# Performance work log

Hardware: AMD Instinct MI355X
Metric: run time of the kernel (lower is better)

## Reference

```python
import jax, jax.numpy as jnp
import numpy as np

N_NODES = 50000

def _sage_conv(x, src, dst, W_l, b_l, W_r):
    # mean-aggregate neighbor features: messages x[src] summed into dst
    msgs = x[src]                                   # [E, d]
    agg = jax.ops.segment_sum(msgs, dst, num_segments=N_NODES)  # [N, d]
    ones = jnp.ones((src.shape[0],), dtype=x.dtype)
    cnt = jax.ops.segment_sum(ones, dst, num_segments=N_NODES)  # [N]
    agg = agg / jnp.maximum(cnt, 1.0)[:, None]
    return agg @ W_l + b_l + x @ W_r


def setup_inputs() -> dict:
    key = jax.random.key(0)
    ks = jax.random.split(key, 8)
    d_in, hid, out = 64, 128, 64
    x = jax.random.normal(ks[0], (N_NODES, d_in), dtype=jnp.float32)
    edge_index = jax.random.randint(ks[1], (2, 1600000), 0, N_NODES, dtype=jnp.int64)
    def w(k, a, b):
        return jax.random.normal(k, (a, b), dtype=jnp.float32) / np.sqrt(a)
    return {
        "x": x,
        "edge_index": edge_index,
        "W_l1": w(ks[2], d_in, hid), "b_l1": jnp.zeros((hid,), jnp.float32),
        "W_r1": w(ks[3], d_in, hid),
        "W_l2": w(ks[4], hid, hid), "b_l2": jnp.zeros((hid,), jnp.float32),
        "W_r2": w(ks[5], hid, hid),
        "W_out": w(ks[6], hid, out), "b_out": jnp.zeros((out,), jnp.float32),
    }


def reference(x, edge_index, W_l1, b_l1, W_r1, W_l2, b_l2, W_r2, W_out, b_out):
    src, dst = edge_index[0], edge_index[1]
    h = jax.nn.relu(_sage_conv(x, src, dst, W_l1, b_l1, W_r1))
    h = jax.nn.relu(_sage_conv(h, src, dst, W_l2, b_l2, W_r2))
    return h @ W_out + b_out
```

## Files before the change

### kernel.cpp

```cpp
#include <hip/hip_runtime.h>


typedef unsigned short ushort_t;
typedef unsigned int uint_t;
typedef unsigned char uchar_t;
typedef __attribute__((ext_vector_type(8))) short short8;
typedef __attribute__((ext_vector_type(8))) ushort_t ushort8;
typedef __attribute__((ext_vector_type(4))) float f32x4;

#define BKT_SHIFT 7
#define BKT_NODES 128
#define BKT_CAP   5120
#define EPB       4096
#define QSCALE    32.0f
#define QINV      0.03125f
#define XQSCALE   16.0f

__device__ inline ushort_t bf16_rne(float v) {
    uint_t u = __float_as_uint(v);
    u += 0x7fffu + ((u >> 16) & 1u);
    return (ushort_t)(u >> 16);
}
__device__ inline float bf16_to_f(ushort_t h) {
    return __uint_as_float((uint_t)h << 16);
}


struct WPack {
    const float* srcp[5];
    ushort_t* dstp[5];
    int K[5], N[5], beg[5], end[5];
};

__global__ __launch_bounds__(1024)
void k_work(const int* __restrict__ src, const int* __restrict__ dst,
            uint_t* __restrict__ pairs, int* __restrict__ bcnt, int E, int nbk,
            int bbl, const float* __restrict__ x, ushort_t* __restrict__ xh,
            ushort_t* __restrict__ xl, uchar_t* __restrict__ xq,
            int NS, WPack wp, int total) {
    int tid = threadIdx.x;
    if (blockIdx.x >= bbl) {
        int t = (blockIdx.x - bbl) * 1024 + tid;
        if (t < NS) {
            float v = x[t];
            ushort_t h = bf16_rne(v);
            xh[t] = h;
            xl[t] = bf16_rne(v - bf16_to_f(h));
            int qv = (int)(v * XQSCALE + 128.5f);
            qv = qv < 0 ? 0 : (qv > 255 ? 255 : qv);
            xq[t] = (uchar_t)qv;
            return;
        }
        t -= NS;
        if (t >= total) return;
#pragma unroll
        for (int m = 0; m < 5; ++m) {
            if (t >= wp.beg[m] && t < wp.end[m]) {
                int i = t - wp.beg[m];
                int K = wp.K[m], N = wp.N[m];
                int k = i / N, nn = i % N;
                int NT = N >> 4;
                int kt = k >> 5, bq = (k >> 3) & 3, j = k & 7;
                int nt = nn >> 4, lane = (bq << 4) | (nn & 15);
                int base = (((kt * NT + nt) << 6) + lane) * 8 + j;
                int halfsz = (K >> 5) * NT * 512;
                float v = wp.srcp[m][i];
                ushort_t h = bf16_rne(v);
                wp.dstp[m][base] = h;
                wp.dstp[m][halfsz + base] = bf16_rne(v - bf16_to_f(h));
            }
        }
        return;
    }

    __shared__ int h[4][512];
    int sub = tid & 3;
    for (int i = tid; i < 4 * 512; i += 1024) ((int*)h)[i] = 0;
    __syncthreads();

    int e = blockIdx.x * EPB + tid * 4;
    bool full = (e + 4 <= E);
    int4 d4 = {0, 0, 0, 0}, s4 = {0, 0, 0, 0};
    if (full) {
        d4 = *(const int4*)(dst + e);
        s4 = *(const int4*)(src + e);
        atomicAdd(&h[sub][d4.x >> BKT_SHIFT], 1);
        atomicAdd(&h[sub][d4.y >> BKT_SHIFT], 1);
        atomicAdd(&h[sub][d4.z >> BKT_SHIFT], 1);
        atomicAdd(&h[sub][d4.w >> BKT_SHIFT], 1);
    } else {
        for (int t = e; t < E && t < e + 4; ++t)
            atomicAdd(&h[sub][dst[t] >> BKT_SHIFT], 1);
    }
    __syncthreads();
    for (int i = tid; i < nbk; i += 1024) {
        int c0 = h[0][i], c1 = h[1][i], c2 = h[2][i], c3 = h[3][i];
        int c = c0 + c1 + c2 + c3;
        int bs = c ? atomicAdd(&bcnt[i], c) : 0;
        h[0][i] = bs; h[1][i] = bs + c0; h[2][i] = bs + c0 + c1;
        h[3][i] = bs + c0 + c1 + c2;
    }
    __syncthreads();
    if (full) {
        int dd[4] = {d4.x, d4.y, d4.z, d4.w};
        int ss[4] = {s4.x, s4.y, s4.z, s4.w};
#pragma unroll
        for (int t = 0; t < 4; ++t) {
            int b = dd[t] >> BKT_SHIFT;
            int r = atomicAdd(&h[sub][b], 1);
            pairs[(size_t)b * BKT_CAP + r] =
                (uint_t)(ss[t] & 0xFFFF) | ((uint_t)(dd[t] & (BKT_NODES - 1)) << 16);
        }
    } else {
        for (int t = e; t < E && t < e + 4; ++t) {
            int d = dst[t];
            int b = d >> BKT_SHIFT;
            int r = atomicAdd(&h[sub][b], 1);
            pairs[(size_t)b * BKT_CAP + r] =
                (uint_t)(src[t] & 0xFFFF) | ((uint_t)(d & (BKT_NODES - 1)) << 16);
        }
    }
}


__global__ __launch_bounds__(1024) void k_csr(const uint_t* __restrict__ pairs,
                                              const int* __restrict__ bcnt,
                                              int* __restrict__ off,
                                              ushort_t* __restrict__ col, int n) {
    __shared__ int hist[BKT_NODES];
    __shared__ int s[BKT_NODES];
    __shared__ int cur[BKT_NODES];
    __shared__ int bofs_s;
    int b = blockIdx.x, tid = threadIdx.x;
    if (tid < 64) {
        int p = 0;
        for (int i = tid; i < b; i += 64) p += bcnt[i];
#pragma unroll
        for (int m = 1; m < 64; m <<= 1) p += __shfl_xor(p, m);
        if (tid == 0) bofs_s = p;
    }
    if (tid < BKT_NODES) hist[tid] = 0;
    __syncthreads();
    int bofs = bofs_s;
    int cnt = bcnt[b];
    const uint_t* p = pairs + (size_t)b * BKT_CAP;
    for (int i = tid; i < cnt; i += 1024) atomicAdd(&hist[(p[i] >> 16) & 127], 1);
    __syncthreads();
    int v = (tid < BKT_NODES) ? hist[tid] : 0;
    if (tid < BKT_NODES) s[tid] = v;
    __syncthreads();
    for (int ofs = 1; ofs < BKT_NODES; ofs <<= 1) {
        int t = (tid >= ofs && tid < BKT_NODES) ? s[tid - ofs] : 0;
        __syncthreads();
        if (tid < BKT_NODES) s[tid] += t;
        __syncthreads();
    }
    if (tid < BKT_NODES) {
        int excl = bofs + s[tid] - v;
        int node = b * BKT_NODES + tid;
        if (node <= n) off[node] = excl;
        cur[tid] = excl;
    }
    __syncthreads();
    for (int i = tid; i < cnt; i += 1024) {
        uint_t pk = p[i];
        int pos = atomicAdd(&cur[(pk >> 16) & 127], 1);
        col[pos] = (ushort_t)(pk & 0xFFFF);
    }
}

template <int ROWB>
__device__ inline void gather_u8(const uchar_t* __restrict__ fbase,
                                 const ushort_t* __restrict__ col,
                                 int s0, int s1, int sub,
                                 uint_t (&ae)[4], uint_t (&ao)[4]) {
    constexpr int EPI = 1024 / ROWB;
#pragma unroll
    for (int i = 0; i < 4; ++i) { ae[i] = 0u; ao[i] = 0u; }
    int e = s0;
    for (; e + 4 * EPI <= s1; e += 4 * EPI) {
        int c[4];
        uint4 q[4];
#pragma unroll
        for (int j = 0; j < 4; ++j) c[j] = col[e + j * EPI + sub];
#pragma unroll
        for (int j = 0; j < 4; ++j) q[j] = *(const uint4*)(fbase + (size_t)c[j] * ROWB);
#pragma unroll
        for (int j = 0; j < 4; ++j) {
            const uint_t* u = (const uint_t*)&q[j];
#pragma unroll
            for (int i = 0; i < 4; ++i) {
                ae[i] += u[i] & 0x00FF00FFu;
                ao[i] += (u[i] >> 8) & 0x00FF00FFu;
            }
        }
    }
    for (; e < s1; e += 2 * EPI) {
        int last = s1 - 1;
        int c[2];
        uint_t msk[2];
        uint4 q[2];
#pragma unroll
        for (int j = 0; j < 2; ++j) {
            int idx = e + j * EPI + sub;
            msk[j] = (idx < s1) ? 0xFFFFFFFFu : 0u;
            c[j] = col[min(idx, last)];
        }
#pragma unroll
        for (int j = 0; j < 2; ++j) q[j] = *(const uint4*)(fbase + (size_t)c[j] * ROWB);
#pragma unroll
        for (int j = 0; j < 2; ++j) {
            const uint_t* u = (const uint_t*)&q[j];
#pragma unroll
            for (int i = 0; i < 4; ++i) {
                uint_t um = u[i] & msk[j];
                ae[i] += um & 0x00FF00FFu;
                ao[i] += (um >> 8) & 0x00FF00FFu;
            }
        }
    }
}

__device__ inline f32x4 mfma3(f32x4 acc, short8 ah, short8 al, short8 bh, short8 bl) {
    acc = __builtin_amdgcn_mfma_f32_16x16x32_bf16(ah, bh, acc, 0, 0, 0);
    acc = __builtin_amdgcn_mfma_f32_16x16x32_bf16(al, bh, acc, 0, 0, 0);
    acc = __builtin_amdgcn_mfma_f32_16x16x32_bf16(ah, bl, acc, 0, 0, 0);
    return acc;
}


__global__ __launch_bounds__(512)
void k_layer1(const uchar_t* __restrict__ xq, const ushort_t* __restrict__ xh,
              const ushort_t* __restrict__ xl,
              const int* __restrict__ off, const ushort_t* __restrict__ col,
              const ushort_t* __restrict__ Wlp, const ushort_t* __restrict__ Wrp,
              const float* __restrict__ bias, ushort_t* __restrict__ Oh,
              uchar_t* __restrict__ Oq, int n) {
    __shared__ ushort_t Ahs[32][72];
    __shared__ ushort_t Als[32][72];
    int tid = threadIdx.x, waveid = tid >> 6, lane = tid & 63;
    int base = blockIdx.x * 32;
    int li = lane & 3;
    int sub = lane >> 2;
    const uchar_t* fbase = xq + li * 16;

    for (int q = 0; q < 4; ++q) {
        int node = base + waveid * 4 + q;
        int nd = node < n ? node : n - 1;
        int s0 = off[nd], s1 = off[nd + 1];
        uint_t ae[4], ao[4];
        gather_u8<64>(fbase, col, s0, s1, sub, ae, ao);
#pragma unroll
        for (int m = 4; m < 64; m <<= 1) {
#pragma unroll
            for (int i = 0; i < 4; ++i) {
                ae[i] += __shfl_xor(ae[i], m);
                ao[i] += __shfl_xor(ao[i], m);
            }
        }
        if (sub == 0) {
            int deg = s1 - s0;
            float inv = 1.f / (XQSCALE * fmaxf((float)deg, 1.f));
            float c8 = deg > 0 ? 8.f : 0.f;
            ushort_t vh[16], vl[16];
#pragma unroll
            for (int i = 0; i < 4; ++i) {
                uint_t f[4] = {ae[i] & 0xFFFFu, ao[i] & 0xFFFFu,
                               ae[i] >> 16, ao[i] >> 16};
#pragma unroll
                for (int b = 0; b < 4; ++b) {
                    float mval = (float)f[b] * inv - c8;
                    ushort_t h = bf16_rne(mval);
                    vh[i * 4 + b] = h;
                    vl[i * 4 + b] = bf16_rne(mval - bf16_to_f(h));
                }
            }
            int r = waveid * 4 + q;
            *(ushort8*)&Ahs[r][li * 16] = *(ushort8*)&vh[0];
            *(ushort8*)&Ahs[r][li * 16 + 8] = *(ushort8*)&vh[8];
            *(ushort8*)&Als[r][li * 16] = *(ushort8*)&vl[0];
            *(ushort8*)&Als[r][li * 16 + 8] = *(ushort8*)&vl[8];
        }
    }
    __syncthreads();

    int rowt = waveid >> 2, c0 = waveid & 3;
    int colq = lane & 15, quad = lane >> 4;
    int arow = rowt * 16 + colq;
    short8 fah[2], fal[2], fxh[2], fxl[2];
#pragma unroll
    for (int kt = 0; kt < 2; ++kt) {
        fah[kt] = *(const short8*)&Ahs[arow][kt * 32 + quad * 8];
        fal[kt] = *(const short8*)&Als[arow][kt * 32 + quad * 8];
    }
    int grow = base + arow; if (grow >= n) grow = n - 1;
#pragma unroll
    for (int kt = 0; kt < 2; ++kt) {
        fxh[kt] = *(const short8*)(xh + (size_t)grow * 64 + kt * 32 + quad * 8);
        fxl[kt] = *(const short8*)(xl + (size_t)grow * 64 + kt * 32 + quad * 8);
    }
#pragma unroll
    for (int t = 0; t < 2; ++t) {
        int nt = c0 + t * 4;
        float bv = bias[nt * 16 + colq];
        f32x4 acc = (f32x4){bv, bv, bv, bv};
#pragma unroll
        for (int kt = 0; kt < 2; ++kt) {
            const ushort_t* pL = Wlp + ((size_t)((kt * 8 + nt) << 6) + lane) * 8;
            acc = mfma3(acc, fah[kt], fal[kt],
                        *(const short8*)pL, *(const short8*)(pL + 8192));
            const ushort_t* pR = Wrp + ((size_t)((kt * 8 + nt) << 6) + lane) * 8;
            acc = mfma3(acc, fxh[kt], fxl[kt],
                        *(const short8*)pR, *(const short8*)(pR + 8192));
        }
        int rowb = base + rowt * 16 + quad * 4;
        int cix = nt * 16 + colq;
#pragma unroll
        for (int r = 0; r < 4; ++r) {
            int row = rowb + r;
            if (row < n) {
                float v = fmaxf(acc[r], 0.f);
                Oh[(size_t)row * 128 + cix] = bf16_rne(v);
                int qv = (int)(v * QSCALE + 0.5f);
                Oq[(size_t)row * 128 + cix] = (uchar_t)(qv > 255 ? 255 : qv);
            }
        }
    }
}


#define L2R 136
__global__ __launch_bounds__(256)
void k_layer2(const uchar_t* __restrict__ h1q, const int* __restrict__ off,
              const ushort_t* __restrict__ col, const ushort_t* __restrict__ h1h,
              const ushort_t* __restrict__ Wlp, const ushort_t* __restrict__ Wrp,
              const float* __restrict__ b2, const ushort_t* __restrict__ Wop,
              const float* __restrict__ bo, float* __restrict__ out, int n) {
    __shared__ ushort_t Ah[16][L2R], Al[16][L2R];
    __shared__ ushort_t Hh[16][L2R], Hl[16][L2R];
    int tid = threadIdx.x, waveid = tid >> 6, lane = tid & 63;
    int base = blockIdx.x * 16;
    int li = lane & 7;
    int sub = lane >> 3;
    const uchar_t* fbase = h1q + li * 16;

    for (int q = 0; q < 4; ++q) {
        int node = base + waveid * 4 + q;
        int nd = node < n ? node : n - 1;
        int s0 = off[nd], s1 = off[nd + 1];
        uint_t ae[4], ao[4];
        gather_u8<128>(fbase, col, s0, s1, sub, ae, ao);
#pragma unroll
        for (int m = 8; m < 64; m <<= 1) {
#pragma unroll
            for (int i = 0; i < 4; ++i) {
                ae[i] += __shfl_xor(ae[i], m);
                ao[i] += __shfl_xor(ao[i], m);
            }
        }
        if (sub == 0) {
            float inv = QINV / fmaxf((float)(s1 - s0), 1.f);
            ushort_t vh[16], vl[16];
#pragma unroll
            for (int i = 0; i < 4; ++i) {
                uint_t f[4] = {ae[i] & 0xFFFFu, ao[i] & 0xFFFFu,
                               ae[i] >> 16, ao[i] >> 16};
#pragma unroll
                for (int b = 0; b < 4; ++b) {
                    float mval = (float)f[b] * inv;
                    ushort_t h = bf16_rne(mval);
                    vh[i * 4 + b] = h;
                    vl[i * 4 + b] = bf16_rne(mval - bf16_to_f(h));
                }
            }
            int r = waveid * 4 + q;
            *(ushort8*)&Ah[r][li * 16] = *(ushort8*)&vh[0];
            *(ushort8*)&Ah[r][li * 16 + 8] = *(ushort8*)&vh[8];
            *(ushort8*)&Al[r][li * 16] = *(ushort8*)&vl[0];
            *(ushort8*)&Al[r][li * 16 + 8] = *(ushort8*)&vl[8];
        }
    }
    __syncthreads();

    int colx = lane & 15, quad = lane >> 4;
    int arow = colx;
    int grow = base + arow; if (grow >= n) grow = n - 1;
    short8 gah[4], gal[4], sh[4];
#pragma unroll
    for (int kt = 0; kt < 4; ++kt) {
        gah[kt] = *(const short8*)&Ah[arow][kt * 32 + quad * 8];
        gal[kt] = *(const short8*)&Al[arow][kt * 32 + quad * 8];
        sh[kt]  = *(const short8*)(h1h + (size_t)grow * 128 + kt * 32 + quad * 8);
    }
#pragma unroll
    for (int t = 0; t < 2; ++t) {
        int nt = waveid + t * 4;
        float bv = b2[nt * 16 + colx];
        f32x4 acc = (f32x4){bv, bv, bv, bv};
#pragma unroll
        for (int kt = 0; kt < 4; ++kt) {
            const ushort_t* pL = Wlp + ((size_t)((kt * 8 + nt) << 6) + lane) * 8;
            acc = mfma3(acc, gah[kt], gal[kt],
                        *(const short8*)pL, *(const short8*)(pL + 16384));
            const ushort_t* pR = Wrp + ((size_t)((kt * 8 + nt) << 6) + lane) * 8;
            short8 bh = *(const short8*)pR;
            short8 bl = *(const short8*)(pR + 16384);
            acc = __builtin_amdgcn_mfma_f32_16x16x32_bf16(sh[kt], bh, acc, 0, 0, 0);
            acc = __builtin_amdgcn_mfma_f32_16x16x32_bf16(sh[kt], bl, acc, 0, 0, 0);
        }
#pragma unroll
        for (int r = 0; r < 4; ++r) {
            int row = quad * 4 + r;
            float v = fmaxf(acc[r], 0.f);
            ushort_t h = bf16_rne(v);
            Hh[row][nt * 16 + colx] = h;
            Hl[row][nt * 16 + colx] = bf16_rne(v - bf16_to_f(h));
        }
    }
    __syncthreads();

    short8 hh[4], hl[4];
#pragma unroll
    for (int kt = 0; kt < 4; ++kt) {
        hh[kt] = *(const short8*)&Hh[arow][kt * 32 + quad * 8];
        hl[kt] = *(const short8*)&Hl[arow][kt * 32 + quad * 8];
    }
    int nt2 = waveid;
    float bv = bo[nt2 * 16 + colx];
    f32x4 acc2 = (f32x4){bv, bv, bv, bv};
#pragma unroll
    for (int kt = 0; kt < 4; ++kt) {
        const ushort_t* p = Wop + ((size_t)((kt * 4 + nt2) << 6) + lane) * 8;
        acc2 = mfma3(acc2, hh[kt], hl[kt],
                     *(const short8*)p, *(const short8*)(p + 8192));
    }
#pragma unroll
    for (int r = 0; r < 4; ++r) {
        int row = base + quad * 4 + r;
        if (row < n) out[(size_t)row * 64 + nt2 * 16 + colx] = acc2[r];
    }
}


static inline size_t align256(size_t x) { return (x + 255) & ~(size_t)255; }

extern "C" void kernel_launch(void* const* d_in, const int* in_sizes, int n_in,
                              void* d_out, int out_size, void* d_ws, size_t ws_size,
                              hipStream_t stream) {
    const float* x   = (const float*)d_in[0];
    const int*   ei  = (const int*)d_in[1];
    const float* Wl1 = (const float*)d_in[2];
    const float* bl1 = (const float*)d_in[3];
    const float* Wr1 = (const float*)d_in[4];
    const float* Wl2 = (const float*)d_in[5];
    const float* bl2 = (const float*)d_in[6];
    const float* Wr2 = (const float*)d_in[7];
    const float* Wo  = (const float*)d_in[8];
    const float* bo  = (const float*)d_in[9];

    const int N = in_sizes[0] / 64;
    const int E = in_sizes[1] / 2;
    const int* src = ei;
    const int* dst = ei + E;
    const int nbk = (N + BKT_NODES - 1) >> BKT_SHIFT;

    char* ws = (char*)d_ws;
    int* off = (int*)ws;            ws += align256((size_t)(N + 1) * 4);
    int* bcnt = (int*)ws;           ws += align256((size_t)nbk * 4);
    uint_t* pairs = (uint_t*)ws;    ws += align256((size_t)nbk * BKT_CAP * 4);
    ushort_t* col = (ushort_t*)ws;  ws += align256((size_t)E * 2);
    ushort_t* xh  = (ushort_t*)ws;  ws += align256((size_t)N * 64 * 2);
    ushort_t* xl  = (ushort_t*)ws;  ws += align256((size_t)N * 64 * 2);
    uchar_t*  xq  = (uchar_t*)ws;   ws += align256((size_t)N * 64);
    ushort_t* h1h = (ushort_t*)ws;  ws += align256((size_t)N * 128 * 2);
    uchar_t*  h1q = (uchar_t*)ws;   ws += align256((size_t)N * 128);
    ushort_t* Wl1p = (ushort_t*)ws; ws += align256((size_t)2 * 64 * 128 * 2);
    ushort_t* Wr1p = (ushort_t*)ws; ws += align256((size_t)2 * 64 * 128 * 2);
    ushort_t* Wl2p = (ushort_t*)ws; ws += align256((size_t)2 * 128 * 128 * 2);
    ushort_t* Wr2p = (ushort_t*)ws; ws += align256((size_t)2 * 128 * 128 * 2);
    ushort_t* Wop  = (ushort_t*)ws; ws += align256((size_t)2 * 128 * 64 * 2);

    WPack wp;
    wp.srcp[0] = Wl1; wp.dstp[0] = Wl1p; wp.K[0] = 64;  wp.N[0] = 128;
    wp.srcp[1] = Wr1; wp.dstp[1] = Wr1p; wp.K[1] = 64;  wp.N[1] = 128;
    wp.srcp[2] = Wl2; wp.dstp[2] = Wl2p; wp.K[2] = 128; wp.N[2] = 128;
    wp.srcp[3] = Wr2; wp.dstp[3] = Wr2p; wp.K[3] = 128; wp.N[3] = 128;
    wp.srcp[4] = Wo;  wp.dstp[4] = Wop;  wp.K[4] = 128; wp.N[4] = 64;
    int acc_el = 0;
    for (int m = 0; m < 5; ++m) {
        wp.beg[m] = acc_el; acc_el += wp.K[m] * wp.N[m]; wp.end[m] = acc_el;
    }
    int NS = N * 64;

    hipMemsetAsync(bcnt, 0, (size_t)nbk * 4, stream);
    int bbl = (E + EPB - 1) / EPB;
    int pbl = (NS + acc_el + 1023) / 1024;
    k_work<<<bbl + pbl, 1024, 0, stream>>>(src, dst, pairs, bcnt, E, nbk, bbl,
                                           x, xh, xl, xq, NS, wp, acc_el);

    k_csr<<<nbk, 1024, 0, stream>>>(pairs, bcnt, off, col, N);

    k_layer1<<<(N + 31) / 32, 512, 0, stream>>>(xq, xh, xl, off, col, Wl1p,
                                                Wr1p, bl1, h1h, h1q, N);

    k_layer2<<<(N + 15) / 16, 256, 0, stream>>>(h1q, off, col, h1h, Wl2p, Wr2p,
                                                bl2, Wop, bo, (float*)d_out, N);
}
```

Measured before the change: 216.8 us.

## Split layer-2 gather into two 64-wide feature-half passes over separate buffers

Layer 1 now writes its quantized 8-bit output as two separate 64-column halves. Two new aggregation kernels each gather one half over the CSR neighbours and store packed partial sums to global memory. A separate dense kernel then reads those sums, normalizes by degree, and runs the MFMA layers. Each gather pass touches a smaller per-node feature footprint, which is meant to improve cache locality for the random neighbour reads. The cost is walking the edge list twice, extra kernel launches, and a round trip of the sums through global memory.

```diff
diff --git a/kernel.cpp b/kernel.cpp
--- a/kernel.cpp
+++ b/kernel.cpp
@@ -235,7 +235,7 @@
               const int* __restrict__ off, const ushort_t* __restrict__ col,
               const ushort_t* __restrict__ Wlp, const ushort_t* __restrict__ Wrp,
               const float* __restrict__ bias, ushort_t* __restrict__ Oh,
-              uchar_t* __restrict__ Oq, int n) {
+              uchar_t* __restrict__ OqA, uchar_t* __restrict__ OqB, int n) {
     __shared__ ushort_t Ahs[32][72];
     __shared__ ushort_t Als[32][72];
     int tid = threadIdx.x, waveid = tid >> 6, lane = tid & 63;
@@ -315,6 +315,8 @@
         }
         int rowb = base + rowt * 16 + quad * 4;
         int cix = nt * 16 + colq;
+        uchar_t* Oqh = t ? OqB : OqA;
+        int qix = c0 * 16 + colq;
 #pragma unroll
         for (int r = 0; r < 4; ++r) {
             int row = rowb + r;
@@ -322,17 +324,44 @@
                 float v = fmaxf(acc[r], 0.f);
                 Oh[(size_t)row * 128 + cix] = bf16_rne(v);
                 int qv = (int)(v * QSCALE + 0.5f);
-                Oq[(size_t)row * 128 + cix] = (uchar_t)(qv > 255 ? 255 : qv);
+                Oqh[(size_t)row * 64 + qix] = (uchar_t)(qv > 255 ? 255 : qv);
             }
         }
+    }
+}
+
+
+__global__ __launch_bounds__(256)
+void k_aggh(const uchar_t* __restrict__ fq, const int* __restrict__ off,
+            const ushort_t* __restrict__ col, uint_t* __restrict__ S, int n) {
+    int wave = (int)((blockIdx.x * (unsigned)blockDim.x + threadIdx.x) >> 6);
+    int lane = threadIdx.x & 63;
+    if (wave >= n) return;
+    int li = lane & 3, sub = lane >> 2;
+    int s0 = off[wave], s1 = off[wave + 1];
+    uint_t ae[4], ao[4];
+    gather_u8<64>(fq + li * 16, col, s0, s1, sub, ae, ao);
+#pragma unroll
+    for (int m = 4; m < 64; m <<= 1) {
+#pragma unroll
+        for (int i = 0; i < 4; ++i) {
+            ae[i] += __shfl_xor(ae[i], m);
+            ao[i] += __shfl_xor(ao[i], m);
+        }
+    }
+    if (sub == 0) {
+        uint4 va = {ae[0], ae[1], ae[2], ae[3]};
+        uint4 vo = {ao[0], ao[1], ao[2], ao[3]};
+        *(uint4*)(S + (size_t)wave * 32 + li * 8) = va;
+        *(uint4*)(S + (size_t)wave * 32 + li * 8 + 4) = vo;
     }
 }
 
 
 #define L2R 136
 __global__ __launch_bounds__(256)
-void k_layer2(const uchar_t* __restrict__ h1q, const int* __restrict__ off,
-              const ushort_t* __restrict__ col, const ushort_t* __restrict__ h1h,
+void k_dense2(const uint_t* __restrict__ SA, const uint_t* __restrict__ SB,
+              const int* __restrict__ off, const ushort_t* __restrict__ h1h,
               const ushort_t* __restrict__ Wlp, const ushort_t* __restrict__ Wrp,
               const float* __restrict__ b2, const ushort_t* __restrict__ Wop,
               const float* __restrict__ bo, float* __restrict__ out, int n) {
@@ -340,45 +369,22 @@
     __shared__ ushort_t Hh[16][L2R], Hl[16][L2R];
     int tid = threadIdx.x, waveid = tid >> 6, lane = tid & 63;
     int base = blockIdx.x * 16;
-    int li = lane & 7;
-    int sub = lane >> 3;
-    const uchar_t* fbase = h1q + li * 16;
-
+
+    int j = lane & 31;
+    const uint_t* Sp = (lane < 32) ? SA : SB;
+    int fofs = (lane < 32) ? 0 : 64;
+    int fl = fofs + ((j >> 3) << 4) + ((j & 3) << 2) + ((j >> 2) & 1);
     for (int q = 0; q < 4; ++q) {
         int node = base + waveid * 4 + q;
         int nd = node < n ? node : n - 1;
-        int s0 = off[nd], s1 = off[nd + 1];
-        uint_t ae[4], ao[4];
-        gather_u8<128>(fbase, col, s0, s1, sub, ae, ao);
-#pragma unroll
-        for (int m = 8; m < 64; m <<= 1) {
-#pragma unroll
-            for (int i = 0; i < 4; ++i) {
-                ae[i] += __shfl_xor(ae[i], m);
-                ao[i] += __shfl_xor(ao[i], m);
-            }
-        }
-        if (sub == 0) {
-            float inv = QINV / fmaxf((float)(s1 - s0), 1.f);
-            ushort_t vh[16], vl[16];
-#pragma unroll
-            for (int i = 0; i < 4; ++i) {
-                uint_t f[4] = {ae[i] & 0xFFFFu, ao[i] & 0xFFFFu,
-                               ae[i] >> 16, ao[i] >> 16};
-#pragma unroll
-                for (int b = 0; b < 4; ++b) {
-                    float mval = (float)f[b] * inv;
-                    ushort_t h = bf16_rne(mval);
-                    vh[i * 4 + b] = h;
-                    vl[i * 4 + b] = bf16_rne(mval - bf16_to_f(h));
-                }
-            }
-            int r = waveid * 4 + q;
-            *(ushort8*)&Ah[r][li * 16] = *(ushort8*)&vh[0];
-            *(ushort8*)&Ah[r][li * 16 + 8] = *(ushort8*)&vh[8];
-            *(ushort8*)&Al[r][li * 16] = *(ushort8*)&vl[0];
-            *(ushort8*)&Al[r][li * 16 + 8] = *(ushort8*)&vl[8];
-        }
+        float inv = QINV / fmaxf((float)(off[nd + 1] - off[nd]), 1.f);
+        uint_t s = Sp[(size_t)nd * 32 + j];
+        float v0 = (float)(s & 0xFFFFu) * inv;
+        float v1 = (float)(s >> 16) * inv;
+        ushort_t h0 = bf16_rne(v0), h1v = bf16_rne(v1);
+        int row = waveid * 4 + q;
+        Ah[row][fl] = h0;      Al[row][fl] = bf16_rne(v0 - bf16_to_f(h0));
+        Ah[row][fl + 2] = h1v; Al[row][fl + 2] = bf16_rne(v1 - bf16_to_f(h1v));
     }
     __syncthreads();
 
@@ -473,7 +479,10 @@
     ushort_t* xl  = (ushort_t*)ws;  ws += align256((size_t)N * 64 * 2);
     uchar_t*  xq  = (uchar_t*)ws;   ws += align256((size_t)N * 64);
     ushort_t* h1h = (ushort_t*)ws;  ws += align256((size_t)N * 128 * 2);
-    uchar_t*  h1q = (uchar_t*)ws;   ws += align256((size_t)N * 128);
+    uchar_t*  h1qA = (uchar_t*)ws;  ws += align256((size_t)N * 64);
+    uchar_t*  h1qB = (uchar_t*)ws;  ws += align256((size_t)N * 64);
+    uint_t*   SA  = (uint_t*)ws;    ws += align256((size_t)N * 32 * 4);
+    uint_t*   SB  = (uint_t*)ws;    ws += align256((size_t)N * 32 * 4);
     ushort_t* Wl1p = (ushort_t*)ws; ws += align256((size_t)2 * 64 * 128 * 2);
     ushort_t* Wr1p = (ushort_t*)ws; ws += align256((size_t)2 * 64 * 128 * 2);
     ushort_t* Wl2p = (ushort_t*)ws; ws += align256((size_t)2 * 128 * 128 * 2);
@@ -501,8 +510,12 @@
     k_csr<<<nbk, 1024, 0, stream>>>(pairs, bcnt, off, col, N);
 
     k_layer1<<<(N + 31) / 32, 512, 0, stream>>>(xq, xh, xl, off, col, Wl1p,
-                                                Wr1p, bl1, h1h, h1q, N);
-
-    k_layer2<<<(N + 15) / 16, 256, 0, stream>>>(h1q, off, col, h1h, Wl2p, Wr2p,
+                                                Wr1p, bl1, h1h, h1qA, h1qB, N);
+
+    int aggbl = (N * 64 + 255) / 256;
+    k_aggh<<<aggbl, 256, 0, stream>>>(h1qA, off, col, SA, N);
+    k_aggh<<<aggbl, 256, 0, stream>>>(h1qB, off, col, SB, N);
+
+    k_dense2<<<(N + 15) / 16, 256, 0, stream>>>(SA, SB, off, h1h, Wl2p, Wr2p,
                                                 bl2, Wop, bo, (float*)d_out, N);
 }
```

New measurement: 233.0 us. +7.5%, slower.
